# Kernel optimization log

Measured on AMD Instinct MI355X. Metric: run time of the kernel, lower is better.

Reference implementation:

```python
import jax, jax.numpy as jnp
import numpy as np

H = 8
D = 512
DK = D // H
B = 16
N = 8192


def setup_inputs() -> dict:
    key = jax.random.key(0)
    k1, k2, k3, k4 = jax.random.split(key, 4)
    x = jax.random.normal(k1, (B, N, D), dtype=jnp.float32)
    W_k = jax.random.normal(k2, (D, D), dtype=jnp.float32) * (1.0 / np.sqrt(D))
    W_g = jax.random.normal(k3, (D, D), dtype=jnp.float32) * (1.0 / np.sqrt(D))
    query = jax.random.normal(k4, (H, 1, DK), dtype=jnp.float32)
    return {"x": x, "W_k": W_k, "W_g": W_g, "query": query}


def reference(x, W_k, W_g, query):
    b, n, d = x.shape
    # nn.Linear: y = x @ W.T  (no bias)
    K = (x @ W_k.T).reshape(b, n, H, DK).transpose(0, 2, 1, 3)  # (b,h,n,dk)
    G = (x @ W_g.T).reshape(b, n, H, DK).transpose(0, 2, 1, 3)  # (b,h,n,dk)
    xh = x.reshape(b, n, H, DK).transpose(0, 2, 1, 3)           # (b,h,n,dk)
    gated = jnp.tanh(K) * jax.nn.sigmoid(G)                     # (b,h,n,dk)
    # single-query attention: scores (b,h,1,n)
    scores = jnp.einsum('hmd,bhnd->bhmn', query, gated)
    attn = jax.nn.softmax(scores, axis=-1)
    out = jnp.einsum('bhmn,bhnd->bhmd', attn, xh)               # (b,h,1,dk)
    out = out.transpose(0, 2, 1, 3).reshape(b, 1, H * DK)
    return out.squeeze()  # (b, d)
```

## Files before the change

kernel.cpp:

```cpp
#include <hip/hip_runtime.h>
#include <hip/hip_bf16.h>

#define H_ 8
#define D_ 512
#define DK_ 64
#define B_ 16
#define N_ 8192
#define M_ (B_ * N_)

typedef __attribute__((ext_vector_type(8))) short short8;
typedef __attribute__((ext_vector_type(4))) float floatx4;

__device__ __forceinline__ void glds16(const void* g, void* l) {
    __builtin_amdgcn_global_load_lds((const __attribute__((address_space(1))) void*)g,
                                     (__attribute__((address_space(3))) void*)l,
                                     16, 0, 0);
}

__device__ __forceinline__ unsigned short f2bf(float f) {
    unsigned u = __float_as_uint(f);
    return (unsigned short)((u + 0x7fffu + ((u >> 16) & 1u)) >> 16);
}

__device__ __forceinline__ unsigned pack_bf2(float x, float y) {
    return __builtin_amdgcn_perm(__float_as_uint(y) + 0x8000u,
                                 __float_as_uint(x) + 0x8000u, 0x07060302u);
}

__device__ __forceinline__ short8 pack_bf8(float4 lo, float4 hi) {
    union { unsigned u[4]; short8 s; } tmp;
    tmp.u[0] = pack_bf2(lo.x, lo.y);
    tmp.u[1] = pack_bf2(lo.z, lo.w);
    tmp.u[2] = pack_bf2(hi.x, hi.y);
    tmp.u[3] = pack_bf2(hi.z, hi.w);
    return tmp.s;
}

__global__ __launch_bounds__(256) void cvt_kernel(const float* __restrict__ src,
                                                  unsigned short* __restrict__ dst, int n4) {
    int i = blockIdx.x * blockDim.x + threadIdx.x;
    int stride = gridDim.x * blockDim.x;
    for (; i < n4; i += stride) {
        float4 v = ((const float4*)src)[i];
        ushort4 o;
        o.x = f2bf(v.x); o.y = f2bf(v.y); o.z = f2bf(v.z); o.w = f2bf(v.w);
        ((ushort4*)dst)[i] = o;
    }
}

__global__ __launch_bounds__(256, 2) void gemm_score_kernel(
    const float* __restrict__ x,
    const unsigned short* __restrict__ wkb,
    const unsigned short* __restrict__ wgb,
    const float* __restrict__ query,
    float* __restrict__ s_buf)
{
    __shared__ unsigned short lds_a[128 * 64];
    __shared__ unsigned short lds_k[128 * 64];
    __shared__ unsigned short lds_g[128 * 64];

    const int t = threadIdx.x;
    const int lane = t & 63;
    const int wave = t >> 6;
    const int wm = wave >> 1, wn = wave & 1;

    const int g = blockIdx.x;
    const int xcd = g & 7;
    const int s = g >> 3;
    const int jt = s & 3;
    const int mt = ((s >> 2) << 3) | xcd;
    const int jc = jt * 128;
    const int m0 = mt * 128;

    floatx4 acc_k[4][4], acc_g[4][4];
#pragma unroll
    for (int i = 0; i < 4; ++i)
#pragma unroll
        for (int j = 0; j < 4; ++j) { acc_k[i][j] = (floatx4)0.f; acc_g[i][j] = (floatx4)0.f; }

    const int r0 = t >> 2;
    const int c0 = t & 3;
    const int swr = ((r0 & 1) << 2) ^ ((r0 >> 1) & 3);
    const float* pA0 = x + (size_t)(m0 + r0) * 512 + c0 * 8;
    const float* pA1 = pA0 + 64 * 512;
    unsigned short* wA00 = lds_a + ((r0 * 8) + (c0 ^ swr)) * 8;
    unsigned short* wA01 = lds_a + ((r0 * 8) + ((c0 ^ swr) ^ 4)) * 8;
    unsigned short* wA10 = wA00 + 64 * 64;
    unsigned short* wA11 = wA01 + 64 * 64;

    int boff[4];
#pragma unroll
    for (int i = 0; i < 4; ++i) {
        int p = i * 256 + t;
        int r = p >> 3;
        int c = (p & 7) ^ (((r & 1) << 2) ^ ((r >> 1) & 3));
        boff[i] = (jc + r) * 512 + c * 8;
    }

    const int fr = lane & 15;
    const int q  = lane >> 4;
    const int swf = ((fr & 1) << 2) ^ ((fr >> 1) & 3);

    for (int k0 = 0; k0 < 512; k0 += 64) {
#pragma unroll
        for (int i = 0; i < 4; ++i) {
            glds16(wkb + boff[i] + k0, lds_k + (size_t)(i * 256 + t) * 8);
            glds16(wgb + boff[i] + k0, lds_g + (size_t)(i * 256 + t) * 8);
        }
        float4 a00 = *(const float4*)(pA0 + k0);
        float4 a01 = *(const float4*)(pA0 + k0 + 4);
        float4 a02 = *(const float4*)(pA0 + k0 + 32);
        float4 a03 = *(const float4*)(pA0 + k0 + 36);
        float4 a10 = *(const float4*)(pA1 + k0);
        float4 a11 = *(const float4*)(pA1 + k0 + 4);
        float4 a12 = *(const float4*)(pA1 + k0 + 32);
        float4 a13 = *(const float4*)(pA1 + k0 + 36);
        *(short8*)wA00 = pack_bf8(a00, a01);
        *(short8*)wA01 = pack_bf8(a02, a03);
        *(short8*)wA10 = pack_bf8(a10, a11);
        *(short8*)wA11 = pack_bf8(a12, a13);
        __syncthreads();

#pragma unroll
        for (int kc = 0; kc < 2; ++kc) {
            const int sl = ((kc * 4 + q) ^ swf) * 8;
            short8 a[4], bk[4], bg[4];
#pragma unroll
            for (int mi = 0; mi < 4; ++mi)
                a[mi] = *(const short8*)(lds_a + (wm * 64 + mi * 16 + fr) * 64 + sl);
#pragma unroll
            for (int ni = 0; ni < 4; ++ni) {
                bk[ni] = *(const short8*)(lds_k + (wn * 64 + ni * 16 + fr) * 64 + sl);
                bg[ni] = *(const short8*)(lds_g + (wn * 64 + ni * 16 + fr) * 64 + sl);
            }
#pragma unroll
            for (int mi = 0; mi < 4; ++mi)
#pragma unroll
                for (int ni = 0; ni < 4; ++ni) {
                    acc_k[mi][ni] = __builtin_amdgcn_mfma_f32_16x16x32_bf16(a[mi], bk[ni], acc_k[mi][ni], 0, 0, 0);
                    acc_g[mi][ni] = __builtin_amdgcn_mfma_f32_16x16x32_bf16(a[mi], bg[ni], acc_g[mi][ni], 0, 0, 0);
                }
        }
        __syncthreads();
    }

    const int h = jt * 2 + wn;
    float qv[4];
#pragma unroll
    for (int ni = 0; ni < 4; ++ni) qv[ni] = query[h * 64 + ni * 16 + fr];

#pragma unroll
    for (int mi = 0; mi < 4; ++mi) {
#pragma unroll
        for (int r = 0; r < 4; ++r) {
            float v = 0.f;
#pragma unroll
            for (int ni = 0; ni < 4; ++ni) {
                float kv = acc_k[mi][ni][r];
                float gv = acc_g[mi][ni][r];
                float e2k = __expf(2.f * kv);
                float th = 1.f - 2.f / (e2k + 1.f);
                float sg = 1.f / (1.f + __expf(-gv));
                v += qv[ni] * th * sg;
            }
            v += __shfl_xor(v, 1);
            v += __shfl_xor(v, 2);
            v += __shfl_xor(v, 4);
            v += __shfl_xor(v, 8);
            if (fr == 0) {
                int mg = m0 + wm * 64 + mi * 16 + (lane >> 4) * 4 + r;
                int b = mg >> 13, n = mg & 8191;
                s_buf[((size_t)(b * 8 + h) << 13) + n] = v;
            }
        }
    }
}

__global__ __launch_bounds__(256) void stats_kernel(const float* __restrict__ s_buf,
                                                    float* __restrict__ mb, float* __restrict__ lb) {
    const int bh = blockIdx.x;
    const float* s = s_buf + ((size_t)bh << 13);
    const int t = threadIdx.x;
    float mx = -3.0e38f;
    for (int i = t; i < 8192; i += 256) mx = fmaxf(mx, s[i]);
#pragma unroll
    for (int m = 32; m > 0; m >>= 1) mx = fmaxf(mx, __shfl_xor(mx, m));
    __shared__ float red[8];
    if ((t & 63) == 0) red[t >> 6] = mx;
    __syncthreads();
    mx = fmaxf(fmaxf(red[0], red[1]), fmaxf(red[2], red[3]));
    float sum = 0.f;
    for (int i = t; i < 8192; i += 256) sum += __expf(s[i] - mx);
#pragma unroll
    for (int m = 32; m > 0; m >>= 1) sum += __shfl_xor(sum, m);
    if ((t & 63) == 0) red[4 + (t >> 6)] = sum;
    __syncthreads();
    if (t == 0) { mb[bh] = mx; lb[bh] = red[4] + red[5] + red[6] + red[7]; }
}

__global__ __launch_bounds__(256) void out_kernel(
    const float* __restrict__ x, const float* __restrict__ s_buf,
    const float* __restrict__ mb, const float* __restrict__ lb,
    float* __restrict__ out) {
    const int b = blockIdx.x >> 5;
    const int chunk = blockIdx.x & 31;
    const int n0 = chunk * 256;
    const int t = threadIdx.x;
    __shared__ float w[8 * 256];
    for (int i = t; i < 2048; i += 256) {
        int hh = i >> 8, nn = i & 255;
        int bh = b * 8 + hh;
        w[i] = __expf(s_buf[((size_t)bh << 13) + n0 + nn] - mb[bh]) / lb[bh];
    }
    __syncthreads();
    const int rg = t >> 6;
    const int d0 = (t & 63) * 8;
    const float* wh = w + ((d0 >> 6) << 8);
    float acc[8] = {0.f, 0.f, 0.f, 0.f, 0.f, 0.f, 0.f, 0.f};
    for (int nn = rg; nn < 256; nn += 4) {
        const float4* row = (const float4*)(x + (((size_t)(b * 8192 + n0 + nn)) << 9) + d0);
        float4 v0 = row[0];
        float4 v1 = row[1];
        float ww = wh[nn];
        acc[0] += ww * v0.x; acc[1] += ww * v0.y;
        acc[2] += ww * v0.z; acc[3] += ww * v0.w;
        acc[4] += ww * v1.x; acc[5] += ww * v1.y;
        acc[6] += ww * v1.z; acc[7] += ww * v1.w;
    }
#pragma unroll
    for (int j = 0; j < 8; ++j) atomicAdd(&out[b * 512 + d0 + j], acc[j]);
}

extern "C" void kernel_launch(void* const* d_in, const int* in_sizes, int n_in,
                              void* d_out, int out_size, void* d_ws, size_t ws_size,
                              hipStream_t stream) {
    const float* x  = (const float*)d_in[0];
    const float* Wk = (const float*)d_in[1];
    const float* Wg = (const float*)d_in[2];
    const float* q  = (const float*)d_in[3];
    float* out = (float*)d_out;

    char* ws = (char*)d_ws;
    unsigned short* wkb = (unsigned short*)ws;
    unsigned short* wgb = (unsigned short*)(ws + 524288ull);
    float* s_buf = (float*)(ws + 1048576ull);
    float* mb = (float*)(ws + 5242880ull);
    float* lb = (float*)(ws + 5243392ull);

    hipMemsetAsync(d_out, 0, 512 * B_ * sizeof(float), stream);

    hipLaunchKernelGGL(cvt_kernel, dim3(256), dim3(256), 0, stream, Wk, wkb, (D_ * D_) / 4);
    hipLaunchKernelGGL(cvt_kernel, dim3(256), dim3(256), 0, stream, Wg, wgb, (D_ * D_) / 4);
    hipLaunchKernelGGL(gemm_score_kernel, dim3(4096), dim3(256), 0, stream, x, wkb, wgb, q, s_buf);
    hipLaunchKernelGGL(stats_kernel, dim3(128), dim3(256), 0, stream, s_buf, mb, lb);
    hipLaunchKernelGGL(out_kernel, dim3(512), dim3(256), 0, stream, x, s_buf, mb, lb, out);
}
```

Measured before the change: 585.0 us.

## Retune GEMM swizzle, fuse gating math, vectorize stats, and reduce out_kernel atomics

Several unrelated changes land together. The fp32-to-bf16 packing now uses the hardware v_cvt_pk_bf16_f32 instruction, and the LDS swizzle becomes a simple row-XOR pattern with a new A-tile load mapping. The tanh*sigmoid epilogue is merged into one reciprocal with clamped exps. stats_kernel reads float4 and keeps the values in registers so s_buf is loaded once. The normalizer is turned into a reciprocal multiply, and out_kernel uses smaller chunks, unrolls by two, and reduces in LDS before issuing 4x fewer atomics. Risks include rounding differences from the packed conversion and the approximate reciprocal.

```diff
diff --git a/kernel.cpp b/kernel.cpp
--- a/kernel.cpp
+++ b/kernel.cpp
@@ -22,17 +22,18 @@
     return (unsigned short)((u + 0x7fffu + ((u >> 16) & 1u)) >> 16);
 }
 
-__device__ __forceinline__ unsigned pack_bf2(float x, float y) {
-    return __builtin_amdgcn_perm(__float_as_uint(y) + 0x8000u,
-                                 __float_as_uint(x) + 0x8000u, 0x07060302u);
+__device__ __forceinline__ unsigned cvt_pk(float lo, float hi) {
+    unsigned r;
+    asm("v_cvt_pk_bf16_f32 %0, %1, %2" : "=v"(r) : "v"(lo), "v"(hi));
+    return r;
 }
 
 __device__ __forceinline__ short8 pack_bf8(float4 lo, float4 hi) {
     union { unsigned u[4]; short8 s; } tmp;
-    tmp.u[0] = pack_bf2(lo.x, lo.y);
-    tmp.u[1] = pack_bf2(lo.z, lo.w);
-    tmp.u[2] = pack_bf2(hi.x, hi.y);
-    tmp.u[3] = pack_bf2(hi.z, hi.w);
+    tmp.u[0] = cvt_pk(lo.x, lo.y);
+    tmp.u[1] = cvt_pk(lo.z, lo.w);
+    tmp.u[2] = cvt_pk(hi.x, hi.y);
+    tmp.u[3] = cvt_pk(hi.z, hi.w);
     return tmp.s;
 }
 
@@ -55,14 +56,17 @@
     const float* __restrict__ query,
     float* __restrict__ s_buf)
 {
-    __shared__ unsigned short lds_a[128 * 64];
-    __shared__ unsigned short lds_k[128 * 64];
-    __shared__ unsigned short lds_g[128 * 64];
+    __shared__ __attribute__((aligned(16))) unsigned short lds_a[128 * 64];
+    __shared__ __attribute__((aligned(16))) unsigned short lds_k[128 * 64];
+    __shared__ __attribute__((aligned(16))) unsigned short lds_g[128 * 64];
 
     const int t = threadIdx.x;
     const int lane = t & 63;
     const int wave = t >> 6;
     const int wm = wave >> 1, wn = wave & 1;
+    const int fr = lane & 15;
+    const int q4 = lane >> 4;
+    const int sw = fr & 7;
 
     const int g = blockIdx.x;
     const int xcd = g & 7;
@@ -72,34 +76,25 @@
     const int jc = jt * 128;
     const int m0 = mt * 128;
 
-    floatx4 acc_k[4][4], acc_g[4][4];
-#pragma unroll
-    for (int i = 0; i < 4; ++i)
-#pragma unroll
-        for (int j = 0; j < 4; ++j) { acc_k[i][j] = (floatx4)0.f; acc_g[i][j] = (floatx4)0.f; }
-
-    const int r0 = t >> 2;
-    const int c0 = t & 3;
-    const int swr = ((r0 & 1) << 2) ^ ((r0 >> 1) & 3);
-    const float* pA0 = x + (size_t)(m0 + r0) * 512 + c0 * 8;
-    const float* pA1 = pA0 + 64 * 512;
-    unsigned short* wA00 = lds_a + ((r0 * 8) + (c0 ^ swr)) * 8;
-    unsigned short* wA01 = lds_a + ((r0 * 8) + ((c0 ^ swr) ^ 4)) * 8;
-    unsigned short* wA10 = wA00 + 64 * 64;
-    unsigned short* wA11 = wA01 + 64 * 64;
+    const int ar = t >> 3;
+    const int ac = t & 7;
+    const float* pA = x + (size_t)(m0 + ar) * 512 + ac * 8;
+    const int awoff = ar * 64 + (ac ^ (ar & 7)) * 8;
 
     int boff[4];
 #pragma unroll
     for (int i = 0; i < 4; ++i) {
         int p = i * 256 + t;
         int r = p >> 3;
-        int c = (p & 7) ^ (((r & 1) << 2) ^ ((r >> 1) & 3));
+        int c = (p & 7) ^ (r & 7);
         boff[i] = (jc + r) * 512 + c * 8;
     }
 
-    const int fr = lane & 15;
-    const int q  = lane >> 4;
-    const int swf = ((fr & 1) << 2) ^ ((fr >> 1) & 3);
+    floatx4 acc_k[4][4], acc_g[4][4];
+#pragma unroll
+    for (int i = 0; i < 4; ++i)
+#pragma unroll
+        for (int j = 0; j < 4; ++j) { acc_k[i][j] = (floatx4)0.f; acc_g[i][j] = (floatx4)0.f; }
 
     for (int k0 = 0; k0 < 512; k0 += 64) {
 #pragma unroll
@@ -107,31 +102,31 @@
             glds16(wkb + boff[i] + k0, lds_k + (size_t)(i * 256 + t) * 8);
             glds16(wgb + boff[i] + k0, lds_g + (size_t)(i * 256 + t) * 8);
         }
-        float4 a00 = *(const float4*)(pA0 + k0);
-        float4 a01 = *(const float4*)(pA0 + k0 + 4);
-        float4 a02 = *(const float4*)(pA0 + k0 + 32);
-        float4 a03 = *(const float4*)(pA0 + k0 + 36);
-        float4 a10 = *(const float4*)(pA1 + k0);
-        float4 a11 = *(const float4*)(pA1 + k0 + 4);
-        float4 a12 = *(const float4*)(pA1 + k0 + 32);
-        float4 a13 = *(const float4*)(pA1 + k0 + 36);
-        *(short8*)wA00 = pack_bf8(a00, a01);
-        *(short8*)wA01 = pack_bf8(a02, a03);
-        *(short8*)wA10 = pack_bf8(a10, a11);
-        *(short8*)wA11 = pack_bf8(a12, a13);
+        float4 av[8];
+#pragma unroll
+        for (int it = 0; it < 4; ++it) {
+            const float* p = pA + (size_t)it * (32 * 512) + k0;
+            av[it * 2]     = *(const float4*)(p);
+            av[it * 2 + 1] = *(const float4*)(p + 4);
+        }
+#pragma unroll
+        for (int it = 0; it < 4; ++it)
+            *(short8*)&lds_a[it * (32 * 64) + awoff] = pack_bf8(av[it * 2], av[it * 2 + 1]);
         __syncthreads();
 
 #pragma unroll
         for (int kc = 0; kc < 2; ++kc) {
-            const int sl = ((kc * 4 + q) ^ swf) * 8;
             short8 a[4], bk[4], bg[4];
 #pragma unroll
-            for (int mi = 0; mi < 4; ++mi)
-                a[mi] = *(const short8*)(lds_a + (wm * 64 + mi * 16 + fr) * 64 + sl);
+            for (int mi = 0; mi < 4; ++mi) {
+                int off = (wm * 64 + mi * 16 + fr) * 64 + (q4 ^ sw) * 8;
+                a[mi] = *(const short8*)&lds_a[off ^ (kc * 32)];
+            }
 #pragma unroll
             for (int ni = 0; ni < 4; ++ni) {
-                bk[ni] = *(const short8*)(lds_k + (wn * 64 + ni * 16 + fr) * 64 + sl);
-                bg[ni] = *(const short8*)(lds_g + (wn * 64 + ni * 16 + fr) * 64 + sl);
+                int off = (wn * 64 + ni * 16 + fr) * 64 + (q4 ^ sw) * 8;
+                bk[ni] = *(const short8*)&lds_k[off ^ (kc * 32)];
+                bg[ni] = *(const short8*)&lds_g[off ^ (kc * 32)];
             }
 #pragma unroll
             for (int mi = 0; mi < 4; ++mi)
@@ -158,17 +153,18 @@
             for (int ni = 0; ni < 4; ++ni) {
                 float kv = acc_k[mi][ni][r];
                 float gv = acc_g[mi][ni][r];
-                float e2k = __expf(2.f * kv);
-                float th = 1.f - 2.f / (e2k + 1.f);
-                float sg = 1.f / (1.f + __expf(-gv));
-                v += qv[ni] * th * sg;
+                float e2k = fminf(__expf(2.f * kv), 1e18f);
+                float eg  = fminf(__expf(gv),      1e18f);
+                float num = (e2k - 1.f) * eg;
+                float den = (e2k + 1.f) * (eg + 1.f);
+                v += qv[ni] * num * __builtin_amdgcn_rcpf(den);
             }
             v += __shfl_xor(v, 1);
             v += __shfl_xor(v, 2);
             v += __shfl_xor(v, 4);
             v += __shfl_xor(v, 8);
             if (fr == 0) {
-                int mg = m0 + wm * 64 + mi * 16 + (lane >> 4) * 4 + r;
+                int mg = m0 + wm * 64 + mi * 16 + q4 * 4 + r;
                 int b = mg >> 13, n = mg & 8191;
                 s_buf[((size_t)(b * 8 + h) << 13) + n] = v;
             }
@@ -179,10 +175,16 @@
 __global__ __launch_bounds__(256) void stats_kernel(const float* __restrict__ s_buf,
                                                     float* __restrict__ mb, float* __restrict__ lb) {
     const int bh = blockIdx.x;
-    const float* s = s_buf + ((size_t)bh << 13);
+    const float4* s4 = (const float4*)(s_buf + ((size_t)bh << 13));
     const int t = threadIdx.x;
+    float4 vv[8];
     float mx = -3.0e38f;
-    for (int i = t; i < 8192; i += 256) mx = fmaxf(mx, s[i]);
+#pragma unroll
+    for (int i = 0; i < 8; ++i) {
+        float4 v = s4[t + i * 256];
+        vv[i] = v;
+        mx = fmaxf(mx, fmaxf(fmaxf(v.x, v.y), fmaxf(v.z, v.w)));
+    }
 #pragma unroll
     for (int m = 32; m > 0; m >>= 1) mx = fmaxf(mx, __shfl_xor(mx, m));
     __shared__ float red[8];
@@ -190,45 +192,68 @@
     __syncthreads();
     mx = fmaxf(fmaxf(red[0], red[1]), fmaxf(red[2], red[3]));
     float sum = 0.f;
-    for (int i = t; i < 8192; i += 256) sum += __expf(s[i] - mx);
+#pragma unroll
+    for (int i = 0; i < 8; ++i) {
+        float4 v = vv[i];
+        sum += __expf(v.x - mx) + __expf(v.y - mx) + __expf(v.z - mx) + __expf(v.w - mx);
+    }
 #pragma unroll
     for (int m = 32; m > 0; m >>= 1) sum += __shfl_xor(sum, m);
     if ((t & 63) == 0) red[4 + (t >> 6)] = sum;
     __syncthreads();
-    if (t == 0) { mb[bh] = mx; lb[bh] = red[4] + red[5] + red[6] + red[7]; }
+    if (t == 0) { mb[bh] = mx; lb[bh] = 1.f / (red[4] + red[5] + red[6] + red[7]); }
 }
 
 __global__ __launch_bounds__(256) void out_kernel(
     const float* __restrict__ x, const float* __restrict__ s_buf,
     const float* __restrict__ mb, const float* __restrict__ lb,
     float* __restrict__ out) {
-    const int b = blockIdx.x >> 5;
-    const int chunk = blockIdx.x & 31;
-    const int n0 = chunk * 256;
+    const int b = blockIdx.x >> 6;
+    const int chunk = blockIdx.x & 63;
+    const int n0 = chunk * 128;
     const int t = threadIdx.x;
-    __shared__ float w[8 * 256];
-    for (int i = t; i < 2048; i += 256) {
-        int hh = i >> 8, nn = i & 255;
+    __shared__ float w[8 * 128];
+    __shared__ float red[3 * 512];
+    for (int i = t; i < 1024; i += 256) {
+        int hh = i >> 7, nn = i & 127;
         int bh = b * 8 + hh;
-        w[i] = __expf(s_buf[((size_t)bh << 13) + n0 + nn] - mb[bh]) / lb[bh];
+        w[i] = __expf(s_buf[((size_t)bh << 13) + n0 + nn] - mb[bh]) * lb[bh];
     }
     __syncthreads();
     const int rg = t >> 6;
     const int d0 = (t & 63) * 8;
-    const float* wh = w + ((d0 >> 6) << 8);
+    const float* wh = w + ((d0 >> 6) << 7);
+    const float* xb = x + (((size_t)(b * 8192 + n0)) << 9) + d0;
     float acc[8] = {0.f, 0.f, 0.f, 0.f, 0.f, 0.f, 0.f, 0.f};
-    for (int nn = rg; nn < 256; nn += 4) {
-        const float4* row = (const float4*)(x + (((size_t)(b * 8192 + n0 + nn)) << 9) + d0);
-        float4 v0 = row[0];
-        float4 v1 = row[1];
-        float ww = wh[nn];
-        acc[0] += ww * v0.x; acc[1] += ww * v0.y;
-        acc[2] += ww * v0.z; acc[3] += ww * v0.w;
-        acc[4] += ww * v1.x; acc[5] += ww * v1.y;
-        acc[6] += ww * v1.z; acc[7] += ww * v1.w;
-    }
-#pragma unroll
-    for (int j = 0; j < 8; ++j) atomicAdd(&out[b * 512 + d0 + j], acc[j]);
+    for (int i = 0; i < 32; i += 2) {
+        const int n1 = rg + i * 4;
+        const int n2 = n1 + 4;
+        const float4* r1p = (const float4*)(xb + ((size_t)n1 << 9));
+        const float4* r2p = (const float4*)(xb + ((size_t)n2 << 9));
+        float4 a0 = r1p[0];
+        float4 a1 = r1p[1];
+        float4 b0 = r2p[0];
+        float4 b1 = r2p[1];
+        float w1 = wh[n1];
+        float w2 = wh[n2];
+        acc[0] += w1 * a0.x; acc[1] += w1 * a0.y; acc[2] += w1 * a0.z; acc[3] += w1 * a0.w;
+        acc[4] += w1 * a1.x; acc[5] += w1 * a1.y; acc[6] += w1 * a1.z; acc[7] += w1 * a1.w;
+        acc[0] += w2 * b0.x; acc[1] += w2 * b0.y; acc[2] += w2 * b0.z; acc[3] += w2 * b0.w;
+        acc[4] += w2 * b1.x; acc[5] += w2 * b1.y; acc[6] += w2 * b1.z; acc[7] += w2 * b1.w;
+    }
+    if (rg != 0) {
+#pragma unroll
+        for (int j = 0; j < 8; ++j) red[(rg - 1) * 512 + (t & 63) * 8 + j] = acc[j];
+    }
+    __syncthreads();
+    if (rg == 0) {
+#pragma unroll
+        for (int j = 0; j < 8; ++j) {
+            float v = acc[j] + red[(t & 63) * 8 + j] + red[512 + (t & 63) * 8 + j]
+                    + red[1024 + (t & 63) * 8 + j];
+            atomicAdd(&out[b * 512 + d0 + j], v);
+        }
+    }
 }
 
 extern "C" void kernel_launch(void* const* d_in, const int* in_sizes, int n_in,
@@ -253,5 +278,5 @@
     hipLaunchKernelGGL(cvt_kernel, dim3(256), dim3(256), 0, stream, Wg, wgb, (D_ * D_) / 4);
     hipLaunchKernelGGL(gemm_score_kernel, dim3(4096), dim3(256), 0, stream, x, wkb, wgb, q, s_buf);
     hipLaunchKernelGGL(stats_kernel, dim3(128), dim3(256), 0, stream, s_buf, mb, lb);
-    hipLaunchKernelGGL(out_kernel, dim3(512), dim3(256), 0, stream, x, s_buf, mb, lb, out);
-}
+    hipLaunchKernelGGL(out_kernel, dim3(1024), dim3(256), 0, stream, x, s_buf, mb, lb, out);
+}
```

Measured after the change: 550.0 us. 1.06x faster.
